# Performance work log

Measured on AMD Instinct MI355X. Metric: run time of the kernel, lower is better.

The kernel has to match this reference:

```python
import jax, jax.numpy as jnp
import numpy as np

TEMPERATURE = 1.0
TINY = np.finfo(np.float32).tiny


def setup_inputs() -> dict:
    key = jax.random.key(0)
    ks = jax.random.split(key, 8)
    B, D, H, K, OUT = 2048, 1024, 512, 32, 2
    s = lambda *sh: 1.0 / np.sqrt(sh[0])
    return {
        "x": jax.random.normal(ks[0], (B, D), jnp.float32),
        "uniform": jax.random.uniform(ks[1], (B, K, D), jnp.float32, TINY, 1.0),
        "w0": jax.random.normal(ks[2], (D, H), jnp.float32) * s(D),
        "b0": jnp.zeros((H,), jnp.float32),
        "w1": jax.random.normal(ks[3], (H, H), jnp.float32) * s(H),
        "b1": jnp.zeros((H,), jnp.float32),
        "wout": jax.random.normal(ks[4], (H, D), jnp.float32) * s(H),
        "bout": jnp.zeros((D,), jnp.float32),
        "wp0": jax.random.normal(ks[5], (D, H), jnp.float32) * s(D),
        "bp0": jnp.zeros((H,), jnp.float32),
        "wp1": jax.random.normal(ks[6], (H, OUT), jnp.float32) * s(H),
        "bp1": jnp.zeros((OUT,), jnp.float32),
        "k": K,
    }


def reference(x, uniform, w0, b0, w1, b1, wout, bout, wp0, bp0, wp1, bp1, k):
    # Selector MLP: relu hidden layers, softmax output over the d features.
    h = jax.nn.relu(x @ w0 + b0)
    h = jax.nn.relu(h @ w1 + b1)
    logits = jax.nn.softmax(h @ wout + bout, axis=-1)  # [B, D]

    # create_mask, training branch: Gumbel-softmax concrete relaxation.
    # uniform: [B, K, D]; gumbel = -log(-log(u))
    gumbel = -jnp.log(-jnp.log(uniform))
    noisy = (gumbel + logits[:, None, :]) / TEMPERATURE  # [B, K, D]
    samples = jax.nn.softmax(noisy, axis=-1)
    masks = jnp.max(samples, axis=1)  # [B, D]

    # Predictor MLP on masked inputs (stands in for the saved model).
    new_inputs = x * masks
    hp = jax.nn.relu(new_inputs @ wp0 + bp0)
    deep_out = hp @ wp1 + bp1  # [B, 2]
    return deep_out, masks
```

## Files before the change

kernel.cpp:

```cpp
#include <hip/hip_runtime.h>

#define BB 2048
#define DD 1024
#define HH 512
#define KK 32

#define AS_GLOBAL __attribute__((address_space(1)))
#define AS_LDS    __attribute__((address_space(3)))

typedef __attribute__((ext_vector_type(8))) short short8;
typedef __attribute__((ext_vector_type(4))) float floatx4;

__device__ __forceinline__ float bf2f(unsigned short u) {
    union { unsigned int u; float f; } c; c.u = ((unsigned int)u) << 16; return c.f;
}
__device__ __forceinline__ unsigned short f2bf(float f) {
    union { float f; unsigned int u; } c; c.f = f;
    unsigned int u = c.u + 0x7FFFu + ((c.u >> 16) & 1u);
    return (unsigned short)(u >> 16);
}

#define WOFF_XB    ((size_t)0)
#define WOFF_W0T   ((size_t)4194304)
#define WOFF_W1T   ((size_t)5242880)
#define WOFF_WOUTT ((size_t)5767168)
#define WOFF_WP0T  ((size_t)6815744)
#define WOFF_H0    ((size_t)7864320)
#define WOFF_H1    ((size_t)9961472)
#define WOFF_LG    ((size_t)12058624)
#define WOFF_NEWIN ((size_t)20447232)
#define WOFF_HP    ((size_t)24641536)

__global__ __launch_bounds__(256) void prep_kernel(
    const float* __restrict__ x,  const float* __restrict__ w0,
    const float* __restrict__ w1, const float* __restrict__ wout,
    const float* __restrict__ wp0, unsigned short* __restrict__ ws)
{
    const int blk = blockIdx.x;
    if (blk < 1024) {
        unsigned short* xb = ws + WOFF_XB / 2;
        const size_t base = (size_t)blk * 2048 + (size_t)threadIdx.x * 8;
        float4 v0 = *(const float4*)(x + base);
        float4 v1 = *(const float4*)(x + base + 4);
        ushort4 o0, o1;
        o0.x = f2bf(v0.x); o0.y = f2bf(v0.y); o0.z = f2bf(v0.z); o0.w = f2bf(v0.w);
        o1.x = f2bf(v1.x); o1.y = f2bf(v1.y); o1.z = f2bf(v1.z); o1.w = f2bf(v1.w);
        *(ushort4*)(xb + base) = o0;
        *(ushort4*)(xb + base + 4) = o1;
        return;
    }
    const float* src; unsigned short* dst; int Kd, N, t;
    if (blk < 1536)      { src = w0;   dst = ws + WOFF_W0T / 2;   Kd = 1024; N = 512;  t = blk - 1024; }
    else if (blk < 1792) { src = w1;   dst = ws + WOFF_W1T / 2;   Kd = 512;  N = 512;  t = blk - 1536; }
    else if (blk < 2304) { src = wout; dst = ws + WOFF_WOUTT / 2; Kd = 512;  N = 1024; t = blk - 1792; }
    else                 { src = wp0;  dst = ws + WOFF_WP0T / 2;  Kd = 1024; N = 512;  t = blk - 2304; }
    const int ntn = N / 32;
    const int kt = t / ntn, nt = t % ntn;
    __shared__ float tile[32][33];
    const int tx = threadIdx.x & 31, ty = threadIdx.x >> 5;
#pragma unroll
    for (int r = 0; r < 32; r += 8)
        tile[ty + r][tx] = src[(size_t)(kt * 32 + ty + r) * N + nt * 32 + tx];
    __syncthreads();
#pragma unroll
    for (int r = 0; r < 32; r += 8)
        dst[(size_t)(nt * 32 + ty + r) * Kd + kt * 32 + tx] = f2bf(tile[tx][ty + r]);
}

template <int RELU, int OUTBF>
__global__ __launch_bounds__(256) void gemm_mfma(
    const unsigned short* __restrict__ A,
    const unsigned short* __restrict__ BT,
    const float* __restrict__ bias,
    void* __restrict__ Cv, int M, int N, int Kd)
{
    __shared__ __align__(16) unsigned short As[2][4096];
    __shared__ __align__(16) unsigned short Bs[2][4096];
    const int tid = threadIdx.x;
    const int bm = blockIdx.y * 64, bn = blockIdx.x * 64;
    const int wave = tid >> 6, lane = tid & 63;

    floatx4 acc[2][2] = {};

    const int sr = tid >> 3;
    const int skc = (tid & 7) ^ ((tid >> 3) & 7);
    const unsigned short* ga = A  + (size_t)(bm + sr) * Kd + skc * 8;
    const unsigned short* ga2 = ga + (size_t)32 * Kd;
    const unsigned short* gb = BT + (size_t)(bn + sr) * Kd + skc * 8;
    const unsigned short* gb2 = gb + (size_t)32 * Kd;
    const int ldoff = wave * 512;

    const int wm = (wave >> 1) * 32, wn = (wave & 1) * 32;
    const int fr = lane & 15, fq = lane >> 4;
    int ua[2], ub[2];
#pragma unroll
    for (int i = 0; i < 2; ++i) {
        const int ra = wm + i * 16 + fr;
        const int rb = wn + i * 16 + fr;
        ua[i] = ra * 8;  ub[i] = rb * 8;
    }

    const int steps = Kd >> 6;

#define STAGE(buf, k0)                                                              \
    do {                                                                            \
        __builtin_amdgcn_global_load_lds((const AS_GLOBAL void*)(ga + (k0)),        \
            (AS_LDS void*)(&As[buf][0] + ldoff), 16, 0, 0);                         \
        __builtin_amdgcn_global_load_lds((const AS_GLOBAL void*)(ga2 + (k0)),       \
            (AS_LDS void*)(&As[buf][2048] + ldoff), 16, 0, 0);                      \
        __builtin_amdgcn_global_load_lds((const AS_GLOBAL void*)(gb + (k0)),        \
            (AS_LDS void*)(&Bs[buf][0] + ldoff), 16, 0, 0);                         \
        __builtin_amdgcn_global_load_lds((const AS_GLOBAL void*)(gb2 + (k0)),       \
            (AS_LDS void*)(&Bs[buf][2048] + ldoff), 16, 0, 0);                      \
    } while (0)

    STAGE(0, 0);
    __syncthreads();

    for (int s = 0; s < steps; ++s) {
        const int buf = s & 1;
        if (s + 1 < steps) STAGE((s + 1) & 1, (s + 1) << 6);
#pragma unroll
        for (int t = 0; t < 2; ++t) {
            short8 a[2], b[2];
#pragma unroll
            for (int i = 0; i < 2; ++i) {
                const int kc = t * 4 + fq;
                const int eA = (wm + i * 16 + fr) & 7;
                const int eB = (wn + i * 16 + fr) & 7;
                a[i] = *(const short8*)(&As[buf][0] + (size_t)(ua[i] + (kc ^ eA)) * 8);
                b[i] = *(const short8*)(&Bs[buf][0] + (size_t)(ub[i] + (kc ^ eB)) * 8);
            }
            acc[0][0] = __builtin_amdgcn_mfma_f32_16x16x32_bf16(a[0], b[0], acc[0][0], 0, 0, 0);
            acc[0][1] = __builtin_amdgcn_mfma_f32_16x16x32_bf16(a[0], b[1], acc[0][1], 0, 0, 0);
            acc[1][0] = __builtin_amdgcn_mfma_f32_16x16x32_bf16(a[1], b[0], acc[1][0], 0, 0, 0);
            acc[1][1] = __builtin_amdgcn_mfma_f32_16x16x32_bf16(a[1], b[1], acc[1][1], 0, 0, 0);
        }
        __syncthreads();
    }
#undef STAGE

    float* Cf = (float*)Cv;
    unsigned short* Cb = (unsigned short*)Cv;
    const int er = fq * 4, ec = fr;
#pragma unroll
    for (int i = 0; i < 2; ++i)
#pragma unroll
        for (int j = 0; j < 2; ++j) {
            const int col = bn + wn + j * 16 + ec;
            const float bv = bias[col];
#pragma unroll
            for (int r = 0; r < 4; ++r) {
                const int row = bm + wm + i * 16 + er + r;
                float v = acc[i][j][r] + bv;
                if (RELU) v = fmaxf(v, 0.0f);
                if (OUTBF) Cb[(size_t)row * N + col] = f2bf(v);
                else       Cf[(size_t)row * N + col] = v;
            }
        }
}

__device__ __forceinline__ float wave_max(float v) {
#pragma unroll
    for (int o = 32; o; o >>= 1) v = fmaxf(v, __shfl_xor(v, o, 64));
    return v;
}
__device__ __forceinline__ float wave_sum(float v) {
#pragma unroll
    for (int o = 32; o; o >>= 1) v += __shfl_xor(v, o, 64);
    return v;
}

__global__ __launch_bounds__(256) void gumbel_fused(
    const float* __restrict__ lgpre,
    const float* __restrict__ uniform,
    const float* __restrict__ x,
    float* __restrict__ masks,
    unsigned short* __restrict__ newin)
{
    const int wave = threadIdx.x >> 6, lane = threadIdx.x & 63;
    const int b = blockIdx.x * 4 + wave;

    float lp[16];
    const float* lrow = lgpre + (size_t)b * DD;
#pragma unroll
    for (int j = 0; j < 4; ++j)
        *(float4*)(lp + j * 4) = *(const float4*)(lrow + lane * 4 + j * 256);
    float M = -1e30f;
#pragma unroll
    for (int i = 0; i < 16; ++i) M = fmaxf(M, lp[i]);
    M = wave_max(M);
    float S = 0.f;
#pragma unroll
    for (int i = 0; i < 16; ++i) { lp[i] = __expf(lp[i] - M); S += lp[i]; }
    S = wave_sum(S);
    const float invS = 1.0f / S;
    float ep[16];
#pragma unroll
    for (int i = 0; i < 16; ++i) ep[i] = __expf(lp[i] * invS);

    float mk[16] = {0.f,0.f,0.f,0.f,0.f,0.f,0.f,0.f,0.f,0.f,0.f,0.f,0.f,0.f,0.f,0.f};
    const float* up = uniform + (size_t)b * KK * DD;
    for (int k = 0; k < KK; ++k) {
        float sv[16], sloc = 0.f;
#pragma unroll
        for (int j = 0; j < 4; ++j) {
            float4 u4 = *(const float4*)(up + (size_t)k * DD + lane * 4 + j * 256);
            const float uu[4] = {u4.x, u4.y, u4.z, u4.w};
#pragma unroll
            for (int q = 0; q < 4; ++q) {
                const float u = uu[q];
                const float vv = u - 1.0f;
                const float tpoly = -vv * (1.4426950f + vv * (-0.7213475f + vv * 0.4808983f));
                const float tlog  = -__builtin_amdgcn_logf(u);
                const float t = (u > 0.984375f) ? tpoly : tlog;
                const float s = ep[j * 4 + q] * __builtin_amdgcn_rcpf(t);
                sv[j * 4 + q] = s;
                sloc += s;
            }
        }
        const float Sk = wave_sum(sloc);
        const float inv = __builtin_amdgcn_rcpf(Sk);
#pragma unroll
        for (int i = 0; i < 16; ++i) mk[i] = fmaxf(mk[i], sv[i] * inv);
    }

#pragma unroll
    for (int j = 0; j < 4; ++j) {
        const int d = lane * 4 + j * 256;
        float4 xv = *(const float4*)(x + (size_t)b * DD + d);
        float4 mo; mo.x = mk[j*4]; mo.y = mk[j*4+1]; mo.z = mk[j*4+2]; mo.w = mk[j*4+3];
        *(float4*)(masks + (size_t)b * DD + d) = mo;
        ushort4 nb;
        nb.x = f2bf(xv.x * mk[j*4]);   nb.y = f2bf(xv.y * mk[j*4+1]);
        nb.z = f2bf(xv.z * mk[j*4+2]); nb.w = f2bf(xv.w * mk[j*4+3]);
        *(ushort4*)(newin + (size_t)b * DD + d) = nb;
    }
}

__global__ __launch_bounds__(256) void final_kernel(
    const unsigned short* __restrict__ hp, const float* __restrict__ wp1,
    const float* __restrict__ bp1, float* __restrict__ out)
{
    const int wave = threadIdx.x >> 6, lane = threadIdx.x & 63;
    const int row = blockIdx.x * 4 + wave;
    const unsigned short* hrow = hp + (size_t)row * HH;
    float a0 = 0.f, a1 = 0.f;
#pragma unroll
    for (int j = 0; j < 8; ++j) {
        const int k = j * 64 + lane;
        const float h = bf2f(hrow[k]);
        const float2 w = *(const float2*)(wp1 + k * 2);
        a0 += h * w.x; a1 += h * w.y;
    }
    a0 = wave_sum(a0); a1 = wave_sum(a1);
    if (lane == 0) {
        out[row * 2 + 0] = a0 + bp1[0];
        out[row * 2 + 1] = a1 + bp1[1];
    }
}

extern "C" void kernel_launch(void* const* d_in, const int* in_sizes, int n_in,
                              void* d_out, int out_size, void* d_ws, size_t ws_size,
                              hipStream_t stream)
{
    (void)in_sizes; (void)n_in; (void)out_size; (void)ws_size;

    const float* x    = (const float*)d_in[0];
    const float* uni  = (const float*)d_in[1];
    const float* w0   = (const float*)d_in[2];
    const float* b0   = (const float*)d_in[3];
    const float* w1   = (const float*)d_in[4];
    const float* b1   = (const float*)d_in[5];
    const float* wout = (const float*)d_in[6];
    const float* bout = (const float*)d_in[7];
    const float* wp0  = (const float*)d_in[8];
    const float* bp0  = (const float*)d_in[9];
    const float* wp1  = (const float*)d_in[10];
    const float* bp1  = (const float*)d_in[11];

    unsigned char* ws = (unsigned char*)d_ws;
    unsigned short* xb    = (unsigned short*)(ws + WOFF_XB);
    unsigned short* w0T   = (unsigned short*)(ws + WOFF_W0T);
    unsigned short* w1T   = (unsigned short*)(ws + WOFF_W1T);
    unsigned short* woutT = (unsigned short*)(ws + WOFF_WOUTT);
    unsigned short* wp0T  = (unsigned short*)(ws + WOFF_WP0T);
    unsigned short* h0    = (unsigned short*)(ws + WOFF_H0);
    unsigned short* h1    = (unsigned short*)(ws + WOFF_H1);
    float*          lg    = (float*)(ws + WOFF_LG);
    unsigned short* newin = (unsigned short*)(ws + WOFF_NEWIN);
    unsigned short* hp    = (unsigned short*)(ws + WOFF_HP);

    float* out   = (float*)d_out;
    float* masks = out + (size_t)BB * 2;

    prep_kernel<<<2816, 256, 0, stream>>>(x, w0, w1, wout, wp0, (unsigned short*)ws);

    gemm_mfma<1, 1><<<dim3(HH / 64, BB / 64), 256, 0, stream>>>(xb, w0T, b0, h0, BB, HH, DD);
    gemm_mfma<1, 1><<<dim3(HH / 64, BB / 64), 256, 0, stream>>>(h0, w1T, b1, h1, BB, HH, HH);
    gemm_mfma<0, 0><<<dim3(DD / 64, BB / 64), 256, 0, stream>>>(h1, woutT, bout, lg, BB, DD, HH);

    gumbel_fused<<<BB / 4, 256, 0, stream>>>(lg, uni, x, masks, newin);

    gemm_mfma<1, 1><<<dim3(HH / 64, BB / 64), 256, 0, stream>>>(newin, wp0T, bp0, hp, BB, HH, DD);
    final_kernel<<<BB / 4, 256, 0, stream>>>(hp, wp1, bp1, out);
}
```

Measured before the change: 444.8 us.

## Shrink GEMM N-tile to 32 and split Gumbel K-loop across four waves

The GEMM block tile goes from 64x64 to 64x32, which doubles the number of blocks so more CUs are occupied for these small GEMMs. The cost is less reuse of each loaded A tile. The Gumbel kernel now gives one block per batch row, with each wave covering 8 of the 32 samples and prefetching the next uniform row into registers. Per-wave maxima are then combined through LDS. This raises parallelism and memory-level concurrency on the dominant uniform read, but adds a block barrier and more blocks.

```diff
diff --git a/kernel.cpp b/kernel.cpp
--- a/kernel.cpp
+++ b/kernel.cpp
@@ -75,30 +75,27 @@
     void* __restrict__ Cv, int M, int N, int Kd)
 {
     __shared__ __align__(16) unsigned short As[2][4096];
-    __shared__ __align__(16) unsigned short Bs[2][4096];
+    __shared__ __align__(16) unsigned short Bs[2][2048];
     const int tid = threadIdx.x;
-    const int bm = blockIdx.y * 64, bn = blockIdx.x * 64;
+    const int bm = blockIdx.y * 64, bn = blockIdx.x * 32;
     const int wave = tid >> 6, lane = tid & 63;
 
-    floatx4 acc[2][2] = {};
+    floatx4 acc[2] = {};
 
     const int sr = tid >> 3;
     const int skc = (tid & 7) ^ ((tid >> 3) & 7);
-    const unsigned short* ga = A  + (size_t)(bm + sr) * Kd + skc * 8;
+    const unsigned short* ga  = A  + (size_t)(bm + sr) * Kd + skc * 8;
     const unsigned short* ga2 = ga + (size_t)32 * Kd;
-    const unsigned short* gb = BT + (size_t)(bn + sr) * Kd + skc * 8;
-    const unsigned short* gb2 = gb + (size_t)32 * Kd;
+    const unsigned short* gb  = BT + (size_t)(bn + sr) * Kd + skc * 8;
     const int ldoff = wave * 512;
 
-    const int wm = (wave >> 1) * 32, wn = (wave & 1) * 32;
+    const int wm = (wave >> 1) * 32, wn = (wave & 1) * 16;
     const int fr = lane & 15, fq = lane >> 4;
-    int ua[2], ub[2];
-#pragma unroll
-    for (int i = 0; i < 2; ++i) {
-        const int ra = wm + i * 16 + fr;
-        const int rb = wn + i * 16 + fr;
-        ua[i] = ra * 8;  ub[i] = rb * 8;
-    }
+    const int e = fr & 7;
+    int ua[2];
+    ua[0] = (wm + fr) * 8;
+    ua[1] = (wm + 16 + fr) * 8;
+    const int ub = (wn + fr) * 8;
 
     const int steps = Kd >> 6;
 
@@ -110,8 +107,6 @@
             (AS_LDS void*)(&As[buf][2048] + ldoff), 16, 0, 0);                      \
         __builtin_amdgcn_global_load_lds((const AS_GLOBAL void*)(gb + (k0)),        \
             (AS_LDS void*)(&Bs[buf][0] + ldoff), 16, 0, 0);                         \
-        __builtin_amdgcn_global_load_lds((const AS_GLOBAL void*)(gb2 + (k0)),       \
-            (AS_LDS void*)(&Bs[buf][2048] + ldoff), 16, 0, 0);                      \
     } while (0)
 
     STAGE(0, 0);
@@ -122,19 +117,12 @@
         if (s + 1 < steps) STAGE((s + 1) & 1, (s + 1) << 6);
 #pragma unroll
         for (int t = 0; t < 2; ++t) {
-            short8 a[2], b[2];
-#pragma unroll
-            for (int i = 0; i < 2; ++i) {
-                const int kc = t * 4 + fq;
-                const int eA = (wm + i * 16 + fr) & 7;
-                const int eB = (wn + i * 16 + fr) & 7;
-                a[i] = *(const short8*)(&As[buf][0] + (size_t)(ua[i] + (kc ^ eA)) * 8);
-                b[i] = *(const short8*)(&Bs[buf][0] + (size_t)(ub[i] + (kc ^ eB)) * 8);
-            }
-            acc[0][0] = __builtin_amdgcn_mfma_f32_16x16x32_bf16(a[0], b[0], acc[0][0], 0, 0, 0);
-            acc[0][1] = __builtin_amdgcn_mfma_f32_16x16x32_bf16(a[0], b[1], acc[0][1], 0, 0, 0);
-            acc[1][0] = __builtin_amdgcn_mfma_f32_16x16x32_bf16(a[1], b[0], acc[1][0], 0, 0, 0);
-            acc[1][1] = __builtin_amdgcn_mfma_f32_16x16x32_bf16(a[1], b[1], acc[1][1], 0, 0, 0);
+            const int kc = t * 4 + fq;
+            const short8 a0 = *(const short8*)(&As[buf][0] + (size_t)(ua[0] + (kc ^ e)) * 8);
+            const short8 a1 = *(const short8*)(&As[buf][0] + (size_t)(ua[1] + (kc ^ e)) * 8);
+            const short8 bb = *(const short8*)(&Bs[buf][0] + (size_t)(ub    + (kc ^ e)) * 8);
+            acc[0] = __builtin_amdgcn_mfma_f32_16x16x32_bf16(a0, bb, acc[0], 0, 0, 0);
+            acc[1] = __builtin_amdgcn_mfma_f32_16x16x32_bf16(a1, bb, acc[1], 0, 0, 0);
         }
         __syncthreads();
     }
@@ -143,21 +131,19 @@
     float* Cf = (float*)Cv;
     unsigned short* Cb = (unsigned short*)Cv;
     const int er = fq * 4, ec = fr;
-#pragma unroll
-    for (int i = 0; i < 2; ++i)
-#pragma unroll
-        for (int j = 0; j < 2; ++j) {
-            const int col = bn + wn + j * 16 + ec;
-            const float bv = bias[col];
-#pragma unroll
-            for (int r = 0; r < 4; ++r) {
-                const int row = bm + wm + i * 16 + er + r;
-                float v = acc[i][j][r] + bv;
-                if (RELU) v = fmaxf(v, 0.0f);
-                if (OUTBF) Cb[(size_t)row * N + col] = f2bf(v);
-                else       Cf[(size_t)row * N + col] = v;
-            }
+    const int col = bn + wn + ec;
+    const float bv = bias[col];
+#pragma unroll
+    for (int i = 0; i < 2; ++i) {
+#pragma unroll
+        for (int r = 0; r < 4; ++r) {
+            const int row = bm + wm + i * 16 + er + r;
+            float v = acc[i][r] + bv;
+            if (RELU) v = fmaxf(v, 0.0f);
+            if (OUTBF) Cb[(size_t)row * N + col] = f2bf(v);
+            else       Cf[(size_t)row * N + col] = v;
         }
+    }
 }
 
 __device__ __forceinline__ float wave_max(float v) {
@@ -179,7 +165,8 @@
     unsigned short* __restrict__ newin)
 {
     const int wave = threadIdx.x >> 6, lane = threadIdx.x & 63;
-    const int b = blockIdx.x * 4 + wave;
+    const int b = blockIdx.x;
+    __shared__ float lmk[4][1024];
 
     float lp[16];
     const float* lrow = lgpre + (size_t)b * DD;
@@ -200,13 +187,22 @@
     for (int i = 0; i < 16; ++i) ep[i] = __expf(lp[i] * invS);
 
     float mk[16] = {0.f,0.f,0.f,0.f,0.f,0.f,0.f,0.f,0.f,0.f,0.f,0.f,0.f,0.f,0.f,0.f};
-    const float* up = uniform + (size_t)b * KK * DD;
-    for (int k = 0; k < KK; ++k) {
+    const float* up = uniform + (size_t)b * KK * DD + (size_t)wave * DD;
+    float4 ucur[4], unext[4];
+#pragma unroll
+    for (int j = 0; j < 4; ++j)
+        ucur[j] = *(const float4*)(up + lane * 4 + j * 256);
+    for (int kk = 0; kk < 8; ++kk) {
+        if (kk < 7) {
+            const float* upn = up + (size_t)(kk + 1) * 4 * DD;
+#pragma unroll
+            for (int j = 0; j < 4; ++j)
+                unext[j] = *(const float4*)(upn + lane * 4 + j * 256);
+        }
         float sv[16], sloc = 0.f;
 #pragma unroll
         for (int j = 0; j < 4; ++j) {
-            float4 u4 = *(const float4*)(up + (size_t)k * DD + lane * 4 + j * 256);
-            const float uu[4] = {u4.x, u4.y, u4.z, u4.w};
+            const float uu[4] = {ucur[j].x, ucur[j].y, ucur[j].z, ucur[j].w};
 #pragma unroll
             for (int q = 0; q < 4; ++q) {
                 const float u = uu[q];
@@ -223,19 +219,32 @@
         const float inv = __builtin_amdgcn_rcpf(Sk);
 #pragma unroll
         for (int i = 0; i < 16; ++i) mk[i] = fmaxf(mk[i], sv[i] * inv);
+#pragma unroll
+        for (int j = 0; j < 4; ++j) ucur[j] = unext[j];
     }
 
 #pragma unroll
     for (int j = 0; j < 4; ++j) {
-        const int d = lane * 4 + j * 256;
-        float4 xv = *(const float4*)(x + (size_t)b * DD + d);
         float4 mo; mo.x = mk[j*4]; mo.y = mk[j*4+1]; mo.z = mk[j*4+2]; mo.w = mk[j*4+3];
-        *(float4*)(masks + (size_t)b * DD + d) = mo;
-        ushort4 nb;
-        nb.x = f2bf(xv.x * mk[j*4]);   nb.y = f2bf(xv.y * mk[j*4+1]);
-        nb.z = f2bf(xv.z * mk[j*4+2]); nb.w = f2bf(xv.w * mk[j*4+3]);
-        *(ushort4*)(newin + (size_t)b * DD + d) = nb;
-    }
+        *(float4*)(&lmk[wave][lane * 4 + j * 256]) = mo;
+    }
+    __syncthreads();
+    const int d0 = threadIdx.x * 4;
+    const float4 m0 = *(const float4*)(&lmk[0][d0]);
+    const float4 m1 = *(const float4*)(&lmk[1][d0]);
+    const float4 m2 = *(const float4*)(&lmk[2][d0]);
+    const float4 m3 = *(const float4*)(&lmk[3][d0]);
+    float4 mm;
+    mm.x = fmaxf(fmaxf(m0.x, m1.x), fmaxf(m2.x, m3.x));
+    mm.y = fmaxf(fmaxf(m0.y, m1.y), fmaxf(m2.y, m3.y));
+    mm.z = fmaxf(fmaxf(m0.z, m1.z), fmaxf(m2.z, m3.z));
+    mm.w = fmaxf(fmaxf(m0.w, m1.w), fmaxf(m2.w, m3.w));
+    const float4 xv = *(const float4*)(x + (size_t)b * DD + d0);
+    *(float4*)(masks + (size_t)b * DD + d0) = mm;
+    ushort4 nb;
+    nb.x = f2bf(xv.x * mm.x); nb.y = f2bf(xv.y * mm.y);
+    nb.z = f2bf(xv.z * mm.z); nb.w = f2bf(xv.w * mm.w);
+    *(ushort4*)(newin + (size_t)b * DD + d0) = nb;
 }
 
 __global__ __launch_bounds__(256) void final_kernel(
@@ -296,12 +305,12 @@
 
     prep_kernel<<<2816, 256, 0, stream>>>(x, w0, w1, wout, wp0, (unsigned short*)ws);
 
-    gemm_mfma<1, 1><<<dim3(HH / 64, BB / 64), 256, 0, stream>>>(xb, w0T, b0, h0, BB, HH, DD);
-    gemm_mfma<1, 1><<<dim3(HH / 64, BB / 64), 256, 0, stream>>>(h0, w1T, b1, h1, BB, HH, HH);
-    gemm_mfma<0, 0><<<dim3(DD / 64, BB / 64), 256, 0, stream>>>(h1, woutT, bout, lg, BB, DD, HH);
-
-    gumbel_fused<<<BB / 4, 256, 0, stream>>>(lg, uni, x, masks, newin);
-
-    gemm_mfma<1, 1><<<dim3(HH / 64, BB / 64), 256, 0, stream>>>(newin, wp0T, bp0, hp, BB, HH, DD);
+    gemm_mfma<1, 1><<<dim3(HH / 32, BB / 64), 256, 0, stream>>>(xb, w0T, b0, h0, BB, HH, DD);
+    gemm_mfma<1, 1><<<dim3(HH / 32, BB / 64), 256, 0, stream>>>(h0, w1T, b1, h1, BB, HH, HH);
+    gemm_mfma<0, 0><<<dim3(DD / 32, BB / 64), 256, 0, stream>>>(h1, woutT, bout, lg, BB, DD, HH);
+
+    gumbel_fused<<<BB, 256, 0, stream>>>(lg, uni, x, masks, newin);
+
+    gemm_mfma<1, 1><<<dim3(HH / 32, BB / 64), 256, 0, stream>>>(newin, wp0T, bp0, hp, BB, HH, DD);
     final_kernel<<<BB / 4, 256, 0, stream>>>(hp, wp1, bp1, out);
 }
```

Result: faster. 435.0 us (-2.2%).
